# Performance work log

Measured on AMD Instinct MI355X. Metric: run time of the kernel, lower is better.

Reference implementation:

```python
import jax, jax.numpy as jnp
import numpy as np

D_MODEL = 2048
NUM_EXPERTS = 64
TOP_K = 4
N_TOKENS = 16384


def setup_inputs() -> dict:
    key = jax.random.key(0)
    k_u, k_e = jax.random.split(key)
    u = jax.random.normal(k_u, (N_TOKENS, D_MODEL), dtype=jnp.float32)
    # E initialized like torch.randn(d_model, num_experts) * 0.01
    E = jax.random.normal(k_e, (D_MODEL, NUM_EXPERTS), dtype=jnp.float32) * 0.01
    bias = jnp.zeros((NUM_EXPERTS,), dtype=jnp.float32)
    return {"u": u, "E": E, "bias": bias}


def reference(u, E, bias):
    # logits: [N, num_experts]
    logits = u @ E + bias
    scores = jax.nn.softmax(logits, axis=-1)
    # torch.topk returns values sorted descending; lax.top_k matches
    topk_s, topk_i = jax.lax.top_k(scores, TOP_K)
    aux_loss = jnp.sum(jnp.mean(scores, axis=0) ** 2) * NUM_EXPERTS
    return (topk_i, topk_s, scores, aux_loss)
```

## Files before the change

### kernel.cpp

```cpp
#include <hip/hip_runtime.h>
#include <math.h>

#define N_TOK 16384
#define DM    2048
#define NE    64
#define TOPK  4

#define OFF_TI  0
#define OFF_TS  (N_TOK * TOPK)
#define OFF_SC  (2 * N_TOK * TOPK)
#define OFF_AUX (2 * N_TOK * TOPK + N_TOK * NE)

#define TPB 64

#define BK    64
#define NCHK  (DM / BK)
#define KSTR  72
#define UPL   (TPB * KSTR)

#define EH_OFF   1024
#define ET_ELEMS ((size_t)NE * DM)
#define WS_NEED  (EH_OFF + 4 * ET_ELEMS)

typedef short s8v __attribute__((ext_vector_type(8)));
typedef float f4v __attribute__((ext_vector_type(4)));

__device__ __forceinline__ unsigned short bf16_rne(float x) {
  unsigned int b = __float_as_uint(x);
  b += 0x7FFFu + ((b >> 16) & 1u);
  return (unsigned short)(b >> 16);
}

__global__ __launch_bounds__(256) void router_prep(
    const float* __restrict__ E, unsigned short* __restrict__ eh,
    unsigned short* __restrict__ el)
{
  __shared__ float t[32][65];
  const int tid = threadIdx.x;
  const int k0  = blockIdx.x * 32;
#pragma unroll
  for (int i = 0; i < 2; ++i) {
    const int fi = i * 256 + tid;
    const int kk = fi >> 4, ee = (fi & 15) * 4;
    const float4 v = *(const float4*)(E + (size_t)(k0 + kk) * NE + ee);
    t[kk][ee] = v.x; t[kk][ee + 1] = v.y; t[kk][ee + 2] = v.z; t[kk][ee + 3] = v.w;
  }
  __syncthreads();
  const int e = tid >> 2, ks = (tid & 3) * 8;
  unsigned int hw[4], lw[4];
#pragma unroll
  for (int p = 0; p < 4; ++p) {
    unsigned short h[2], l[2];
#pragma unroll
    for (int q = 0; q < 2; ++q) {
      const float x = t[ks + p * 2 + q][e];
      h[q] = bf16_rne(x);
      l[q] = bf16_rne(x - __uint_as_float((unsigned)h[q] << 16));
    }
    hw[p] = (unsigned)h[0] | ((unsigned)h[1] << 16);
    lw[p] = (unsigned)l[0] | ((unsigned)l[1] << 16);
  }
  const size_t o = (size_t)e * DM + k0 + ks;
  *(uint4*)(eh + o) = make_uint4(hw[0], hw[1], hw[2], hw[3]);
  *(uint4*)(el + o) = make_uint4(lw[0], lw[1], lw[2], lw[3]);
}

#define LOAD_U(pf, c) do { _Pragma("unroll") \
  for (int i_ = 0; i_ < 4; ++i_) \
    pf[i_] = *(const float4*)(ugp + (size_t)(c) * BK + i_ * 16); } while (0)

#define WRITE_U(pf, base) do { _Pragma("unroll") \
  for (int i_ = 0; i_ < 4; ++i_) { \
    const float4 v_ = pf[i_]; \
    const unsigned short h0_ = bf16_rne(v_.x), h1_ = bf16_rne(v_.y), \
                         h2_ = bf16_rne(v_.z), h3_ = bf16_rne(v_.w); \
    const unsigned short l0_ = bf16_rne(v_.x - __uint_as_float((unsigned)h0_ << 16)); \
    const unsigned short l1_ = bf16_rne(v_.y - __uint_as_float((unsigned)h1_ << 16)); \
    const unsigned short l2_ = bf16_rne(v_.z - __uint_as_float((unsigned)h2_ << 16)); \
    const unsigned short l3_ = bf16_rne(v_.w - __uint_as_float((unsigned)h3_ << 16)); \
    *(uint2*)&sh[(base) + uoff + i_ * 16] = \
      make_uint2((unsigned)h0_ | ((unsigned)h1_ << 16), (unsigned)h2_ | ((unsigned)h3_ << 16)); \
    *(uint2*)&sh[(base) + UPL + uoff + i_ * 16] = \
      make_uint2((unsigned)l0_ | ((unsigned)l1_ << 16), (unsigned)l2_ | ((unsigned)l3_ << 16)); \
  } } while (0)

#define COMPUTE(c, base) do { _Pragma("unroll") \
  for (int ks_ = 0; ks_ < 2; ++ks_) { \
    const s8v ah_ = *(const s8v*)&sh[(base) + a_off + ks_ * 32]; \
    const s8v al_ = *(const s8v*)&sh[(base) + UPL + a_off + ks_ * 32]; \
    _Pragma("unroll") for (int j_ = 0; j_ < 4; ++j_) { \
      const size_t bo_ = bbase + (size_t)j_ * (16 * DM) + (size_t)(c) * BK + ks_ * 32; \
      const s8v bh_ = *(const s8v*)&eh[bo_]; \
      const s8v bl_ = *(const s8v*)&el[bo_]; \
      acc[j_] = __builtin_amdgcn_mfma_f32_16x16x32_bf16(ah_, bh_, acc[j_], 0, 0, 0); \
      acc[j_] = __builtin_amdgcn_mfma_f32_16x16x32_bf16(ah_, bl_, acc[j_], 0, 0, 0); \
      acc[j_] = __builtin_amdgcn_mfma_f32_16x16x32_bf16(al_, bh_, acc[j_], 0, 0, 0); \
      acc[j_] = __builtin_amdgcn_mfma_f32_16x16x32_bf16(al_, bl_, acc[j_], 0, 0, 0); \
    } } } while (0)

__global__ __launch_bounds__(256, 1) void router_main_mfma(
    const float* __restrict__ u, const unsigned short* __restrict__ eh,
    const unsigned short* __restrict__ el, const float* __restrict__ bias,
    float* __restrict__ out, float* __restrict__ ws)
{
  __shared__ __align__(16) unsigned short sh[4 * UPL];

  const int tid  = threadIdx.x;
  const int lane = tid & 63;
  const int w    = __builtin_amdgcn_readfirstlane(tid >> 6);
  const int lm   = lane & 15;
  const int lk   = lane >> 4;
  const int tok0 = blockIdx.x * TPB;

  const int srow = tid >> 2, sseg = tid & 3;
  const float* ugp = u + (size_t)(tok0 + srow) * DM + sseg * 4;
  const int uoff = srow * KSTR + sseg * 4;

  const int a_off = (w * 16 + lm) * KSTR + lk * 8;
  const size_t bbase = (size_t)lm * DM + lk * 8;

  f4v acc[4];
#pragma unroll
  for (int j = 0; j < 4; ++j) acc[j] = (f4v){0.f, 0.f, 0.f, 0.f};

  float4 pfA[4], pfB[4];
  LOAD_U(pfA, 0);
  LOAD_U(pfB, 1);
  WRITE_U(pfA, 0);
  __syncthreads();

  for (int cc = 0; cc < NCHK; cc += 2) {
    WRITE_U(pfB, 2 * UPL);
    if (cc + 2 < NCHK) LOAD_U(pfA, cc + 2);
    COMPUTE(cc, 0);
    __syncthreads();
    if (cc + 2 < NCHK) WRITE_U(pfA, 0);
    if (cc + 3 < NCHK) LOAD_U(pfB, cc + 3);
    COMPUTE(cc + 1, 2 * UPL);
    __syncthreads();
  }

  float* fin = (float*)sh;
#pragma unroll
  for (int j = 0; j < 4; ++j)
#pragma unroll
    for (int q = 0; q < 4; ++q)
      fin[(w * 16 + lk * 4 + q) * 68 + j * 16 + lm] = acc[j][q];
  __syncthreads();

  const float be = bias[lane];
  float asum = 0.f;
  for (int tt = 0; tt < 16; ++tt) {
    const int t = w * 16 + tt;
    float x = fin[t * 68 + lane] + be;

    float m = x;
#pragma unroll
    for (int off = 32; off > 0; off >>= 1) m = fmaxf(m, __shfl_xor(m, off));
    float p = expf(x - m);
    float s = p;
#pragma unroll
    for (int off = 32; off > 0; off >>= 1) s += __shfl_xor(s, off);
    float sc = p / s;

    out[OFF_SC + (size_t)(tok0 + t) * NE + lane] = sc;
    asum += sc;

    float v = sc;
#pragma unroll
    for (int k = 0; k < TOPK; ++k) {
      float bv = v;
      int   bi = lane;
#pragma unroll
      for (int off = 32; off > 0; off >>= 1) {
        float ov = __shfl_xor(bv, off);
        int   oi = __shfl_xor(bi, off);
        if (ov > bv || (ov == bv && oi < bi)) { bv = ov; bi = oi; }
      }
      if (lane == k) {
        out[OFF_TI + (size_t)(tok0 + t) * TOPK + k] = (float)bi;
        out[OFF_TS + (size_t)(tok0 + t) * TOPK + k] = bv;
      }
      if (lane == bi) v = -INFINITY;
    }
  }
  atomicAdd(&ws[lane], asum);
}

#define FB_DC   32
#define FB_NCH  (1024 / FB_DC)
#define FB_LSTR 68
#define FB_UB   (TPB * FB_LSTR)
#define FB_EOFF (2 * FB_UB)
#define FB_EB   (2 * FB_DC * NE)

__global__ __launch_bounds__(1024, 4) void router_main_fb(
    const float* __restrict__ u, const float* __restrict__ E,
    const float* __restrict__ bias, float* __restrict__ out,
    float* __restrict__ ws)
{
  __shared__ float smem[FB_EOFF + 2 * FB_EB];

  const int tid  = threadIdx.x;
  const int lane = tid & 63;
  const int wid  = __builtin_amdgcn_readfirstlane(tid >> 6);
  const int eg   = wid & 7;
  const int kh   = wid >> 3;
  const int tok0 = blockIdx.x * TPB;

  const int stok  = tid >> 4;
  const int sdseg = tid & 15;
  const int skh   = sdseg >> 3;
  const int sdsub = (sdseg & 7) * 4;
  const float* sgbase = u + (size_t)(tok0 + stok) * DM + skh * 1024 + sdsub;
  float* swp = smem + stok * FB_LSTR + sdseg * 4;

  const int eq  = tid & 511;
  const int ekh = tid >> 9;
  const float* egbase = E + (size_t)ekh * 1024 * NE + eq * 4;
  float* ewp = smem + FB_EOFF + ekh * (FB_DC * NE) + eq * 4;

  float acc[8];
#pragma unroll
  for (int j = 0; j < 8; ++j) acc[j] = 0.f;

  float4 pf[3];
  pf[0] = *(const float4*)(sgbase + 0 * FB_DC);
  pf[1] = *(const float4*)(sgbase + 1 * FB_DC);
  pf[2] = *(const float4*)(sgbase + 2 * FB_DC);
  float4 epf = *(const float4*)(egbase + 0 * (FB_DC * NE));
  *(float4*)(swp + 0) = pf[0];
  *(float4*)(ewp + 0) = epf;
  epf = *(const float4*)(egbase + 1 * (FB_DC * NE));
  __syncthreads();

  for (int c = 0; c < FB_NCH; ++c) {
    if (c + 1 < FB_NCH) {
      *(float4*)(swp + ((c + 1) & 1) * FB_UB) = pf[(c + 1) % 3];
      *(float4*)(ewp + ((c + 1) & 1) * FB_EB) = epf;
    }
    if (c + 2 < FB_NCH)
      epf = *(const float4*)(egbase + (c + 2) * (FB_DC * NE));
    if (c + 3 < FB_NCH)
      pf[c % 3] = *(const float4*)(sgbase + (c + 3) * FB_DC);

    const float* sb = smem + (c & 1) * FB_UB + lane * FB_LSTR + kh * FB_DC;
    const float* eb = smem + FB_EOFF + (c & 1) * FB_EB + kh * (FB_DC * NE) + eg * 8;
#pragma unroll
    for (int s = 0; s < 8; ++s) {
      float4 uf = *(const float4*)(sb + s * 4);
#pragma unroll
      for (int dd = 0; dd < 4; ++dd) {
        const float* er = eb + (s * 4 + dd) * NE;
        float4 e0 = *(const float4*)(er);
        float4 e1 = *(const float4*)(er + 4);
        const float uv = (&uf.x)[dd];
        acc[0] = fmaf(e0.x, uv, acc[0]);
        acc[1] = fmaf(e0.y, uv, acc[1]);
        acc[2] = fmaf(e0.z, uv, acc[2]);
        acc[3] = fmaf(e0.w, uv, acc[3]);
        acc[4] = fmaf(e1.x, uv, acc[4]);
        acc[5] = fmaf(e1.y, uv, acc[5]);
        acc[6] = fmaf(e1.z, uv, acc[6]);
        acc[7] = fmaf(e1.w, uv, acc[7]);
      }
    }
    __syncthreads();
  }

  float* fin = smem;
  if (kh == 0) {
#pragma unroll
    for (int j = 0; j < 8; ++j) fin[lane * 65 + eg * 8 + j] = acc[j];
  }
  __syncthreads();
  if (kh == 1) {
#pragma unroll
    for (int j = 0; j < 8; ++j) fin[lane * 65 + eg * 8 + j] += acc[j];
  }
  __syncthreads();

  const float be = bias[lane];
  float asum = 0.f;
#pragma unroll
  for (int tt = 0; tt < 4; ++tt) {
    const int t = wid * 4 + tt;
    float x = fin[t * 65 + lane] + be;

    float m = x;
#pragma unroll
    for (int off = 32; off > 0; off >>= 1) m = fmaxf(m, __shfl_xor(m, off));
    float p = expf(x - m);
    float s = p;
#pragma unroll
    for (int off = 32; off > 0; off >>= 1) s += __shfl_xor(s, off);
    float sc = p / s;

    out[OFF_SC + (size_t)(tok0 + t) * NE + lane] = sc;
    asum += sc;

    float v = sc;
#pragma unroll
    for (int k = 0; k < TOPK; ++k) {
      float bv = v;
      int   bi = lane;
#pragma unroll
      for (int off = 32; off > 0; off >>= 1) {
        float ov = __shfl_xor(bv, off);
        int   oi = __shfl_xor(bi, off);
        if (ov > bv || (ov == bv && oi < bi)) { bv = ov; bi = oi; }
      }
      if (lane == k) {
        out[OFF_TI + (size_t)(tok0 + t) * TOPK + k] = (float)bi;
        out[OFF_TS + (size_t)(tok0 + t) * TOPK + k] = bv;
      }
      if (lane == bi) v = -INFINITY;
    }
  }
  atomicAdd(&ws[lane], asum);
}

__global__ void router_aux(const float* __restrict__ ws, float* __restrict__ out)
{
  const int lane = threadIdx.x & 63;
  float m = ws[lane] * (1.0f / N_TOK);
  float v = m * m;
#pragma unroll
  for (int off = 32; off > 0; off >>= 1) v += __shfl_xor(v, off);
  if (lane == 0) out[OFF_AUX] = v * (float)NE;
}

extern "C" void kernel_launch(void* const* d_in, const int* in_sizes, int n_in,
                              void* d_out, int out_size, void* d_ws, size_t ws_size,
                              hipStream_t stream) {
  const float* u    = (const float*)d_in[0];
  const float* E    = (const float*)d_in[1];
  const float* bias = (const float*)d_in[2];
  float* out = (float*)d_out;
  float* ws  = (float*)d_ws;

  hipMemsetAsync(ws, 0, NE * sizeof(float), stream);
  if (ws_size >= WS_NEED) {
    unsigned short* eh = (unsigned short*)((char*)ws + EH_OFF);
    unsigned short* el = eh + ET_ELEMS;
    router_prep<<<DM / 32, 256, 0, stream>>>(E, eh, el);
    router_main_mfma<<<N_TOK / TPB, 256, 0, stream>>>(u, eh, el, bias, out, ws);
  } else {
    router_main_fb<<<N_TOK / TPB, 1024, 0, stream>>>(u, E, bias, out, ws);
  }
  router_aux<<<1, 64, 0, stream>>>(ws, out);
}
```

Measured before the change: 315.6 us.

## Split K across waves with 16-token blocks and cross-wave reduction

New measurement: 329.2 us. +4.3%, slower.

```diff
diff --git a/kernel.cpp b/kernel.cpp
--- a/kernel.cpp
+++ b/kernel.cpp
@@ -11,12 +11,11 @@
 #define OFF_SC  (2 * N_TOK * TOPK)
 #define OFF_AUX (2 * N_TOK * TOPK + N_TOK * NE)
 
-#define TPB 64
-
-#define BK    64
-#define NCHK  (DM / BK)
-#define KSTR  72
-#define UPL   (TPB * KSTR)
+#define MTPB  16
+#define RW    256
+#define NRND  (DM / RW)
+#define RSTR  264
+#define PLN   (MTPB * RSTR)
 
 #define EH_OFF   1024
 #define ET_ELEMS ((size_t)NE * DM)
@@ -65,9 +64,9 @@
   *(uint4*)(el + o) = make_uint4(lw[0], lw[1], lw[2], lw[3]);
 }
 
-#define LOAD_U(pf, c) do { _Pragma("unroll") \
+#define LOAD_U(pf, r) do { _Pragma("unroll") \
   for (int i_ = 0; i_ < 4; ++i_) \
-    pf[i_] = *(const float4*)(ugp + (size_t)(c) * BK + i_ * 16); } while (0)
+    pf[i_] = *(const float4*)(ugp + (size_t)(r) * RW + i_ * 64); } while (0)
 
 #define WRITE_U(pf, base) do { _Pragma("unroll") \
   for (int i_ = 0; i_ < 4; ++i_) { \
@@ -78,18 +77,18 @@
     const unsigned short l1_ = bf16_rne(v_.y - __uint_as_float((unsigned)h1_ << 16)); \
     const unsigned short l2_ = bf16_rne(v_.z - __uint_as_float((unsigned)h2_ << 16)); \
     const unsigned short l3_ = bf16_rne(v_.w - __uint_as_float((unsigned)h3_ << 16)); \
-    *(uint2*)&sh[(base) + uoff + i_ * 16] = \
+    *(uint2*)&sh[(base) + uoff + i_ * 64] = \
       make_uint2((unsigned)h0_ | ((unsigned)h1_ << 16), (unsigned)h2_ | ((unsigned)h3_ << 16)); \
-    *(uint2*)&sh[(base) + UPL + uoff + i_ * 16] = \
+    *(uint2*)&sh[(base) + PLN + uoff + i_ * 64] = \
       make_uint2((unsigned)l0_ | ((unsigned)l1_ << 16), (unsigned)l2_ | ((unsigned)l3_ << 16)); \
   } } while (0)
 
-#define COMPUTE(c, base) do { _Pragma("unroll") \
+#define COMPUTE(r, base) do { _Pragma("unroll") \
   for (int ks_ = 0; ks_ < 2; ++ks_) { \
     const s8v ah_ = *(const s8v*)&sh[(base) + a_off + ks_ * 32]; \
-    const s8v al_ = *(const s8v*)&sh[(base) + UPL + a_off + ks_ * 32]; \
+    const s8v al_ = *(const s8v*)&sh[(base) + PLN + a_off + ks_ * 32]; \
     _Pragma("unroll") for (int j_ = 0; j_ < 4; ++j_) { \
-      const size_t bo_ = bbase + (size_t)j_ * (16 * DM) + (size_t)(c) * BK + ks_ * 32; \
+      const size_t bo_ = bbase + (size_t)j_ * (16 * DM) + (size_t)(r) * RW + kq * 64 + ks_ * 32; \
       const s8v bh_ = *(const s8v*)&eh[bo_]; \
       const s8v bl_ = *(const s8v*)&el[bo_]; \
       acc[j_] = __builtin_amdgcn_mfma_f32_16x16x32_bf16(ah_, bh_, acc[j_], 0, 0, 0); \
@@ -98,25 +97,25 @@
       acc[j_] = __builtin_amdgcn_mfma_f32_16x16x32_bf16(al_, bl_, acc[j_], 0, 0, 0); \
     } } } while (0)
 
-__global__ __launch_bounds__(256, 1) void router_main_mfma(
+__global__ __launch_bounds__(256, 4) void router_main_mfma(
     const float* __restrict__ u, const unsigned short* __restrict__ eh,
     const unsigned short* __restrict__ el, const float* __restrict__ bias,
     float* __restrict__ out, float* __restrict__ ws)
 {
-  __shared__ __align__(16) unsigned short sh[4 * UPL];
+  __shared__ __align__(16) unsigned short sh[4 * PLN];
 
   const int tid  = threadIdx.x;
   const int lane = tid & 63;
-  const int w    = __builtin_amdgcn_readfirstlane(tid >> 6);
+  const int kq   = __builtin_amdgcn_readfirstlane(tid >> 6);
   const int lm   = lane & 15;
   const int lk   = lane >> 4;
-  const int tok0 = blockIdx.x * TPB;
-
-  const int srow = tid >> 2, sseg = tid & 3;
+  const int tok0 = blockIdx.x * MTPB;
+
+  const int srow = tid >> 4, sseg = tid & 15;
   const float* ugp = u + (size_t)(tok0 + srow) * DM + sseg * 4;
-  const int uoff = srow * KSTR + sseg * 4;
-
-  const int a_off = (w * 16 + lm) * KSTR + lk * 8;
+  const int uoff = srow * RSTR + sseg * 4;
+
+  const int a_off = lm * RSTR + kq * 64 + lk * 8;
   const size_t bbase = (size_t)lm * DM + lk * 8;
 
   f4v acc[4];
@@ -129,14 +128,14 @@
   WRITE_U(pfA, 0);
   __syncthreads();
 
-  for (int cc = 0; cc < NCHK; cc += 2) {
-    WRITE_U(pfB, 2 * UPL);
-    if (cc + 2 < NCHK) LOAD_U(pfA, cc + 2);
-    COMPUTE(cc, 0);
+  for (int rr = 0; rr < NRND; rr += 2) {
+    WRITE_U(pfB, 2 * PLN);
+    if (rr + 2 < NRND) LOAD_U(pfA, rr + 2);
+    COMPUTE(rr, 0);
     __syncthreads();
-    if (cc + 2 < NCHK) WRITE_U(pfA, 0);
-    if (cc + 3 < NCHK) LOAD_U(pfB, cc + 3);
-    COMPUTE(cc + 1, 2 * UPL);
+    if (rr + 2 < NRND) WRITE_U(pfA, 0);
+    if (rr + 3 < NRND) LOAD_U(pfB, rr + 3);
+    COMPUTE(rr + 1, 2 * PLN);
     __syncthreads();
   }
 
@@ -145,14 +144,16 @@
   for (int j = 0; j < 4; ++j)
 #pragma unroll
     for (int q = 0; q < 4; ++q)
-      fin[(w * 16 + lk * 4 + q) * 68 + j * 16 + lm] = acc[j][q];
+      fin[kq * (16 * 68) + (lk * 4 + q) * 68 + j * 16 + lm] = acc[j][q];
   __syncthreads();
 
   const float be = bias[lane];
   float asum = 0.f;
-  for (int tt = 0; tt < 16; ++tt) {
-    const int t = w * 16 + tt;
-    float x = fin[t * 68 + lane] + be;
+#pragma unroll
+  for (int tt = 0; tt < 4; ++tt) {
+    const int t = kq * 4 + tt;
+    float x = fin[t * 68 + lane] + fin[1 * 1088 + t * 68 + lane]
+            + fin[2 * 1088 + t * 68 + lane] + fin[3 * 1088 + t * 68 + lane] + be;
 
     float m = x;
 #pragma unroll
@@ -187,6 +188,7 @@
   atomicAdd(&ws[lane], asum);
 }
 
+#define TPB     64
 #define FB_DC   32
 #define FB_NCH  (1024 / FB_DC)
 #define FB_LSTR 68
@@ -344,7 +346,7 @@
     unsigned short* eh = (unsigned short*)((char*)ws + EH_OFF);
     unsigned short* el = eh + ET_ELEMS;
     router_prep<<<DM / 32, 256, 0, stream>>>(E, eh, el);
-    router_main_mfma<<<N_TOK / TPB, 256, 0, stream>>>(u, eh, el, bias, out, ws);
+    router_main_mfma<<<N_TOK / MTPB, 256, 0, stream>>>(u, eh, el, bias, out, ws);
   } else {
     router_main_fb<<<N_TOK / TPB, 1024, 0, stream>>>(u, E, bias, out, ws);
   }
```
